# Kernel optimization log

Measured on AMD Instinct MI355X. Metric: run time of the kernel, lower is better.

The kernel has to match this reference:

```python
import jax, jax.numpy as jnp
import numpy as np

T, N, D = 64, 40, 4
H, R, K = 256, 64, 2
E = N * (N - 1)


def _xavier(key, shape):
    std = (2.0 / (shape[0] + shape[1])) ** 0.5
    return (std * jax.random.normal(key, shape)).astype(jnp.float32)


def setup_inputs() -> dict:
    ks = iter(jax.random.split(jax.random.key(0), 40))
    send, recv = np.where(np.ones((N, N)) - np.eye(N))  # fully-connected directed graph, E = N*(N-1)
    p = {}
    p['inputs'] = jax.random.normal(next(ks), (1, T, N, D), dtype=jnp.float32)
    p['node_masks'] = jnp.ones((1, T, N), dtype=jnp.float32)
    p['send_edges'] = jnp.asarray(send, dtype=jnp.int32)
    p['recv_edges'] = jnp.asarray(recv, dtype=jnp.int32)
    for name, nin in (('mlp1', D), ('mlp2', 2 * H), ('mlp3', H), ('mlp4', 3 * H)):
        p[name + '_W1'] = _xavier(next(ks), (H, nin))
        p[name + '_b1'] = jnp.full((H,), 0.1, jnp.float32)
        p[name + '_W2'] = _xavier(next(ks), (H, H))
        p[name + '_b2'] = jnp.full((H,), 0.1, jnp.float32)
    s = float(1.0 / np.sqrt(R))
    for nm in ('fwd', 'rev'):
        p[nm + '_Wih'] = jax.random.uniform(next(ks), (4 * R, H), jnp.float32, -s, s)
        p[nm + '_Whh'] = jax.random.uniform(next(ks), (4 * R, R), jnp.float32, -s, s)
        p[nm + '_bih'] = jnp.zeros((4 * R,), jnp.float32)
        p[nm + '_bhh'] = jnp.zeros((4 * R,), jnp.float32)
    p['enc_W'] = _xavier(next(ks), (K, 2 * R))
    p['enc_b'] = jnp.full((K,), 0.1, jnp.float32)
    p['prior_W'] = _xavier(next(ks), (K, R))
    p['prior_b'] = jnp.full((K,), 0.1, jnp.float32)
    return p


def _mlp(x, W1, b1, W2, b2):
    # RefNRIMLP in eval mode with no_bn=True: elu(fc2(elu(fc1(x))))
    return jax.nn.elu(jax.nn.elu(x @ W1.T + b1) @ W2.T + b2)


def _lstm(xs, Wih, Whh, bih, bhh):
    # xs: [T, E, H] -> hidden states [T, E, R]; PyTorch LSTM gate order i, f, g, o
    def step(carry, xt):
        h, c = carry
        g = xt @ Wih.T + bih + h @ Whh.T + bhh
        i, f, gg, o = jnp.split(g, 4, axis=-1)
        c = jax.nn.sigmoid(f) * c + jax.nn.sigmoid(i) * jnp.tanh(gg)
        h = jax.nn.sigmoid(o) * jnp.tanh(c)
        return (h, c), h
    Rh = Whh.shape[1]
    init = (jnp.zeros((xs.shape[1], Rh), xs.dtype), jnp.zeros((xs.shape[1], Rh), xs.dtype))
    _, hs = jax.lax.scan(step, init, xs)
    return hs


def _encode(inputs, send, recv,
            m1W1, m1b1, m1W2, m1b2, m2W1, m2b1, m2W2, m2b2,
            m3W1, m3b1, m3W2, m3b2, m4W1, m4b1, m4W2, m4b2,
            fWih, fWhh, fbih, fbhh, rWih, rWhh, rbih, rbhh,
            encW, encb, priW, prib):
    x = inputs[0]                                                  # [T, N, D]
    h = _mlp(x, m1W1, m1b1, m1W2, m1b2)                            # [T, N, H]
    e = jnp.concatenate([h[:, send], h[:, recv]], axis=-1)         # node2edge gather [T, E, 2H]
    e = _mlp(e, m2W1, m2b1, m2W2, m2b2)                            # [T, E, H]
    skip = e
    n = jnp.zeros((x.shape[0], x.shape[1], e.shape[-1]), e.dtype)
    n = n.at[:, recv].add(e)                                       # edge2node scatter-add (index_add_)
    n = _mlp(n, m3W1, m3b1, m3W2, m3b2)                            # [T, N, H]
    e = jnp.concatenate([n[:, send], n[:, recv], skip], axis=-1)   # [T, E, 3H]
    e = _mlp(e, m4W1, m4b1, m4W2, m4b2)                            # per-edge features over time [T, E, H]
    fwd_h = _lstm(e, fWih, fWhh, fbih, fbhh)                       # [T, E, R]
    rev_h = _lstm(e[::-1], rWih, rWhh, rbih, rbhh)[::-1]           # [T, E, R]
    prior = fwd_h @ priW.T + prib                                  # [T, E, K]
    enc = jnp.concatenate([fwd_h, rev_h], axis=-1) @ encW.T + encb # [T, E, K]
    return jnp.concatenate([prior, enc], axis=-1)                  # [T, E, 2K]


def reference(inputs, node_masks, send_edges, recv_edges,
              mlp1_W1, mlp1_b1, mlp1_W2, mlp1_b2,
              mlp2_W1, mlp2_b1, mlp2_W2, mlp2_b2,
              mlp3_W1, mlp3_b1, mlp3_W2, mlp3_b2,
              mlp4_W1, mlp4_b1, mlp4_W2, mlp4_b2,
              fwd_Wih, fwd_Whh, fwd_bih, fwd_bhh,
              rev_Wih, rev_Whh, rev_bih, rev_bhh,
              enc_W, enc_b, prior_W, prior_b):
    del node_masks  # all nodes present -> static fully-connected graph each step
    return _encode(inputs, send_edges, recv_edges,
                   mlp1_W1, mlp1_b1, mlp1_W2, mlp1_b2,
                   mlp2_W1, mlp2_b1, mlp2_W2, mlp2_b2,
                   mlp3_W1, mlp3_b1, mlp3_W2, mlp3_b2,
                   mlp4_W1, mlp4_b1, mlp4_W2, mlp4_b2,
                   fwd_Wih, fwd_Whh, fwd_bih, fwd_bhh,
                   rev_Wih, rev_Whh, rev_bih, rev_bhh,
                   enc_W, enc_b, prior_W, prior_b)
```

## Files before the change

kernel.cpp:

```cpp
#include <hip/hip_runtime.h>
#include <math.h>

#define T_ 64
#define N_ 40
#define D_ 4
#define H_ 256
#define R_ 64
#define E_ 1560
#define TE_ (T_*E_)
#define TN_ (T_*N_)

typedef unsigned short us;
typedef short short8 __attribute__((ext_vector_type(8)));
typedef float f32x4 __attribute__((ext_vector_type(4)));

__device__ __forceinline__ float elu_f(float x){ return x > 0.f ? x : (__expf(x) - 1.f); }
__device__ __forceinline__ float sig_f(float x){ return 1.f/(1.f+__expf(-x)); }
__device__ __forceinline__ float tanh_f(float x){ return 2.f/(1.f+__expf(-2.f*x)) - 1.f; }
__device__ __forceinline__ float dot4(float4 a, float4 b){ return a.x*b.x + a.y*b.y + a.z*b.z + a.w*b.w; }

__device__ __forceinline__ float bf2f(us u){ return __uint_as_float(((unsigned int)u) << 16); }
__device__ __forceinline__ us f2bf(float f){
    unsigned int u = __float_as_uint(f);
    u += 0x7FFFu + ((u >> 16) & 1u);
    return (us)(u >> 16);
}
__device__ __forceinline__ float4 ld4f(const float* p){ return *(const float4*)p; }
__device__ __forceinline__ float4 ld4f(const us* p){
    ushort4 v = *(const ushort4*)p;
    return make_float4(bf2f(v.x), bf2f(v.y), bf2f(v.z), bf2f(v.w));
}
__device__ __forceinline__ void st4f(float* p, float4 v){ *(float4*)p = v; }
__device__ __forceinline__ void st4f(us* p, float4 v){
    ushort4 o; o.x = f2bf(v.x); o.y = f2bf(v.y); o.z = f2bf(v.z); o.w = f2bf(v.w);
    *(ushort4*)p = o;
}

__device__ __forceinline__ void gld16(void* lds, const void* g){
    __builtin_amdgcn_global_load_lds((const __attribute__((address_space(1))) unsigned int*)g,
                                     (__attribute__((address_space(3))) unsigned int*)lds,
                                     16, 0, 0);
}

__device__ __forceinline__ void wsplit1(const float* W, us* hi, us* lo, int i){
    const float w = W[i];
    const us h = f2bf(w);
    hi[i] = h;
    lo[i] = f2bf(w - bf2f(h));
}

__global__ __launch_bounds__(256)
void wsplit_all(const float* __restrict__ s0, us* h0, us* l0,
                const float* __restrict__ s1, us* h1, us* l1,
                const float* __restrict__ s2, us* h2, us* l2,
                const float* __restrict__ s3, us* h3, us* l3,
                const float* __restrict__ s4, us* h4, us* l4,
                const float* __restrict__ s5, us* h5, us* l5,
                const float* __restrict__ s6, us* h6, us* l6)
{
    int i = blockIdx.x * 256 + threadIdx.x;
    if (i < 65536) { wsplit1(s0, h0, l0, i); return; } i -= 65536;
    if (i < 65536) {
        const float w = s1[(i >> 8) * 768 + 512 + (i & 255)];
        const us h = f2bf(w);
        h1[i] = h;
        l1[i] = f2bf(w - bf2f(h));
        return;
    } i -= 65536;
    if (i < 65536) { wsplit1(s2, h2, l2, i); return; } i -= 65536;
    if (i < 65536) { wsplit1(s3, h3, l3, i); return; } i -= 65536;
    if (i < 65536) { wsplit1(s4, h4, l4, i); return; } i -= 65536;
    if (i < 16384) { wsplit1(s5, h5, l5, i); return; } i -= 16384;
    wsplit1(s6, h6, l6, i);
}

__global__ __launch_bounds__(256)
void mlp1_kernel(const float* __restrict__ x,
                 const float* __restrict__ W1, const float* __restrict__ b1,
                 const float* __restrict__ W2, const float* __restrict__ b2,
                 us* __restrict__ hout)
{
    __shared__ float xs[8][4];
    __shared__ float h1[8][256];
    const int tid = threadIdx.x;
    const int r0  = blockIdx.x * 8;

    if (tid < 32) xs[tid >> 2][tid & 3] = x[r0 * 4 + tid];
    __syncthreads();

    const float4 w1 = *(const float4*)&W1[tid * 4];
    const float bb1 = b1[tid];
    #pragma unroll
    for (int row = 0; row < 8; ++row) {
        float v = bb1 + xs[row][0]*w1.x + xs[row][1]*w1.y + xs[row][2]*w1.z + xs[row][3]*w1.w;
        h1[row][tid] = elu_f(v);
    }
    __syncthreads();

    float acc[8];
    const float bb2 = b2[tid];
    #pragma unroll
    for (int row = 0; row < 8; ++row) acc[row] = bb2;
    const float* w2row = W2 + (size_t)tid * 256;
    for (int k4 = 0; k4 < 64; ++k4) {
        const float4 w = *(const float4*)&w2row[k4 * 4];
        #pragma unroll
        for (int row = 0; row < 8; ++row) {
            const float4 hh = *(const float4*)&h1[row][k4 * 4];
            acc[row] += dot4(hh, w);
        }
    }
    #pragma unroll
    for (int row = 0; row < 8; ++row)
        hout[(size_t)(r0 + row) * 256 + tid] = f2bf(elu_f(acc[row]));
}

__global__ __launch_bounds__(256)
void node_proj(const us* __restrict__ A, const float* __restrict__ W,
               int wstride, float* __restrict__ P)
{
    __shared__ float As[16][64];
    __shared__ float Ws[16][64];

    const int tid  = threadIdx.x;
    const int am   = tid >> 2;
    const int gm   = blockIdx.x * 64 + am;
    const int part = blockIdx.y >> 2;
    const int wq   = blockIdx.y & 3;

    const us* aptr = A + (size_t)gm * 256;
    const float* wptr = W + (size_t)(wq * 64 + am) * wstride + part * 256;

    const int tx = tid & 15, ty = tid >> 4;
    float acc[4][4] = {};

    for (int k0 = 0; k0 < 256; k0 += 16) {
        const float4 a4 = ld4f(aptr + k0 + (tid & 3) * 4);
        const float4 w4 = *(const float4*)(wptr + k0 + (tid & 3) * 4);

        __syncthreads();
        const int ak = (tid & 3) * 4;
        As[ak+0][am] = a4.x; As[ak+1][am] = a4.y; As[ak+2][am] = a4.z; As[ak+3][am] = a4.w;
        Ws[ak+0][am] = w4.x; Ws[ak+1][am] = w4.y; Ws[ak+2][am] = w4.z; Ws[ak+3][am] = w4.w;
        __syncthreads();

        #pragma unroll
        for (int kq = 0; kq < 16; ++kq) {
            const float4 av = *(const float4*)&As[kq][ty * 4];
            const float4 wv = *(const float4*)&Ws[kq][tx * 4];
            const float a_[4] = {av.x, av.y, av.z, av.w};
            const float w_[4] = {wv.x, wv.y, wv.z, wv.w};
            #pragma unroll
            for (int i = 0; i < 4; ++i)
                #pragma unroll
                for (int j = 0; j < 4; ++j)
                    acc[i][j] += a_[i] * w_[j];
        }
    }

    const int gn = part * 256 + wq * 64 + tx * 4;
    #pragma unroll
    for (int i = 0; i < 4; ++i) {
        const int row = blockIdx.x * 64 + ty * 4 + i;
        float4 o;
        o.x = acc[i][0]; o.y = acc[i][1]; o.z = acc[i][2]; o.w = acc[i][3];
        *(float4*)(P + (size_t)row * 512 + gn) = o;
    }
}

__global__ __launch_bounds__(256)
void edge_gather_elu(const float* __restrict__ P, const float* __restrict__ b1,
                     const int* __restrict__ send, const int* __restrict__ recv,
                     us* __restrict__ out)
{
    const int tid = threadIdx.x;
    const int r   = blockIdx.x * 4 + (tid >> 6);
    const int c4  = (tid & 63) * 4;
    const int t = r / E_;
    const int e = r - t * E_;
    const float4 a  = *(const float4*)(P + ((size_t)(t * N_ + send[e])) * 512 + c4);
    const float4 b  = *(const float4*)(P + ((size_t)(t * N_ + recv[e])) * 512 + 256 + c4);
    const float4 bb = *(const float4*)(b1 + c4);
    float4 v;
    v.x = elu_f(a.x + b.x + bb.x);
    v.y = elu_f(a.y + b.y + bb.y);
    v.z = elu_f(a.z + b.z + bb.z);
    v.w = elu_f(a.w + b.w + bb.w);
    ushort4 o; o.x = f2bf(v.x); o.y = f2bf(v.y); o.z = f2bf(v.z); o.w = f2bf(v.w);
    *(ushort4*)(out + (size_t)r * 256 + c4) = o;
}

template<int MODE, bool DOELU>
__global__ __launch_bounds__(256, 2)
void gemm_mfma(const us* __restrict__ A,
               const us* __restrict__ Whi, const us* __restrict__ Wlo,
               const float* __restrict__ bias1, const float* __restrict__ bias2,
               const int* __restrict__ send, const int* __restrict__ recv,
               const float* __restrict__ Ptab,
               us* __restrict__ C, int Kdim,
               const us* __restrict__ Whi2, const us* __restrict__ Wlo2,
               const float* __restrict__ bias1b, const float* __restrict__ bias2b,
               us* __restrict__ C2)
{
    __shared__ char smem[65536];

    const int tid  = threadIdx.x;
    const int lane = tid & 63;
    const int w    = tid >> 6;
    const int ml   = lane & 15;
    const int q    = lane >> 4;
    const int bx   = blockIdx.x;
    int by         = blockIdx.y;
    const int eh   = w >> 1;
    const int fh   = w & 1;

    if (MODE == 0 && C2 != nullptr && by >= 2) {
        Whi = Whi2; Wlo = Wlo2; bias1 = bias1b; bias2 = bias2b; C = C2; by -= 2;
    }

    const int lr   = lane >> 2;
    const int cofs = (((lane & 3) ^ ((lane >> 3) & 3)) * 8);

    const us* pA0[4];
    #pragma unroll
    for (int i = 0; i < 4; ++i) {
        const int gr = bx * 256 + i * 64 + w * 16 + lr;
        pA0[i] = A + (size_t)gr * Kdim;
    }
    const us *pWh[2], *pWl[2];
    #pragma unroll
    for (int j = 0; j < 2; ++j) {
        const int wr = by * 128 + j * 64 + w * 16 + lr;
        pWh[j] = Whi + (size_t)wr * Kdim;
        pWl[j] = Wlo + (size_t)wr * Kdim;
    }

    f32x4 acc[4][8];
    #pragma unroll
    for (int i = 0; i < 4; ++i)
        #pragma unroll
        for (int j = 0; j < 8; ++j)
            acc[i][j] = (f32x4){0.f, 0.f, 0.f, 0.f};

    auto stage = [&](int k0, char* base) {
        #pragma unroll
        for (int i = 0; i < 4; ++i)
            gld16(base + (i * 4 + w) * 1024, pA0[i] + k0 + cofs);
        #pragma unroll
        for (int j = 0; j < 2; ++j) {
            gld16(base + 16384 + (j * 4 + w) * 1024, pWh[j] + k0 + cofs);
            gld16(base + 24576 + (j * 4 + w) * 1024, pWl[j] + k0 + cofs);
        }
    };

    const int qs16 = (q ^ ((ml >> 1) & 3)) * 16;

    stage(0, smem);
    const int nk = Kdim >> 5;
    for (int k = 0; k < nk; ++k) {
        char* cur = smem + (k & 1) * 32768;
        char* nxt = smem + ((k + 1) & 1) * 32768;
        __builtin_amdgcn_s_barrier();
        if (k + 1 < nk) {
            stage((k + 1) * 32, nxt);
            __builtin_amdgcn_s_waitcnt(0x3F78);
        } else {
            __builtin_amdgcn_s_waitcnt(0x3F70);
        }
        __builtin_amdgcn_s_barrier();

        short8 wh[4], wl[4], ef[8];
        #pragma unroll
        for (int mt = 0; mt < 4; ++mt) {
            const int blkOf = (fh * 4 + mt) * 1024 + ml * 64 + qs16;
            wh[mt] = *(const short8*)(cur + 16384 + blkOf);
            wl[mt] = *(const short8*)(cur + 24576 + blkOf);
        }
        #pragma unroll
        for (int nt = 0; nt < 8; ++nt) {
            const int blkOf = (eh * 8 + nt) * 1024 + ml * 64 + qs16;
            ef[nt] = *(const short8*)(cur + blkOf);
        }
        #pragma unroll
        for (int nt = 0; nt < 8; ++nt)
            #pragma unroll
            for (int mt = 0; mt < 4; ++mt) {
                acc[mt][nt] = __builtin_amdgcn_mfma_f32_16x16x32_bf16(wh[mt], ef[nt], acc[mt][nt], 0, 0, 0);
                acc[mt][nt] = __builtin_amdgcn_mfma_f32_16x16x32_bf16(wl[mt], ef[nt], acc[mt][nt], 0, 0, 0);
            }
    }

    int srowA[8], rrowA[8];
    if (MODE == 3) {
        #pragma unroll
        for (int nt = 0; nt < 8; ++nt) {
            const int row = bx * 256 + eh * 128 + nt * 16 + ml;
            const int t = row / E_;
            const int e = row - t * E_;
            srowA[nt] = t * N_ + send[e];
            rrowA[nt] = t * N_ + recv[e];
        }
    }

    #pragma unroll
    for (int mt = 0; mt < 4; ++mt) {
        const int colb = by * 128 + fh * 64 + mt * 16 + q * 4;
        float4 bb = *(const float4*)(bias1 + colb);
        if (bias2) {
            const float4 b2 = *(const float4*)(bias2 + colb);
            bb.x += b2.x; bb.y += b2.y; bb.z += b2.z; bb.w += b2.w;
        }
        #pragma unroll
        for (int nt = 0; nt < 8; ++nt) {
            const int row = bx * 256 + eh * 128 + nt * 16 + ml;
            float4 v;
            v.x = acc[mt][nt][0] + bb.x; v.y = acc[mt][nt][1] + bb.y;
            v.z = acc[mt][nt][2] + bb.z; v.w = acc[mt][nt][3] + bb.w;
            if (MODE == 3) {
                const float4 pS = *(const float4*)(Ptab + (size_t)srowA[nt] * 512 + colb);
                const float4 pR = *(const float4*)(Ptab + (size_t)rrowA[nt] * 512 + 256 + colb);
                v.x += pS.x + pR.x; v.y += pS.y + pR.y;
                v.z += pS.z + pR.z; v.w += pS.w + pR.w;
            }
            if (DOELU) { v.x = elu_f(v.x); v.y = elu_f(v.y); v.z = elu_f(v.z); v.w = elu_f(v.w); }
            ushort4 o; o.x = f2bf(v.x); o.y = f2bf(v.y); o.z = f2bf(v.z); o.w = f2bf(v.w);
            *(ushort4*)(C + (size_t)row * 256 + colb) = o;
        }
    }
}

template<bool DOELU, typename TA, typename TC>
__global__ __launch_bounds__(256)
void gemm_nt(const TA* __restrict__ A, const float* __restrict__ W,
             const float* __restrict__ bias1,
             TC* __restrict__ C, int M, int Kdim)
{
    __shared__ float As[16][64];
    __shared__ float Ws[16][64];

    const int tid = threadIdx.x;
    const int am  = tid >> 2;
    const int ak  = (tid & 3) * 4;
    const int gm  = blockIdx.x * 64 + am;

    const TA* aptr0 = A + (size_t)gm * Kdim;
    const float* wptr = W + (size_t)(blockIdx.y * 64 + am) * Kdim;

    const int tx = tid & 15, ty = tid >> 4;
    float acc[4][4] = {};

    for (int k0 = 0; k0 < Kdim; k0 += 16) {
        const float4 a4 = ld4f(aptr0 + k0 + ak);
        const float4 w4 = *(const float4*)(wptr + k0 + (tid & 3) * 4);

        __syncthreads();
        As[ak+0][am] = a4.x; As[ak+1][am] = a4.y; As[ak+2][am] = a4.z; As[ak+3][am] = a4.w;
        const int wk = (tid & 3) * 4;
        Ws[wk+0][am] = w4.x; Ws[wk+1][am] = w4.y; Ws[wk+2][am] = w4.z; Ws[wk+3][am] = w4.w;
        __syncthreads();

        #pragma unroll
        for (int kq = 0; kq < 16; ++kq) {
            const float4 av = *(const float4*)&As[kq][ty * 4];
            const float4 wv = *(const float4*)&Ws[kq][tx * 4];
            const float a_[4] = {av.x, av.y, av.z, av.w};
            const float w_[4] = {wv.x, wv.y, wv.z, wv.w};
            #pragma unroll
            for (int i = 0; i < 4; ++i)
                #pragma unroll
                for (int j = 0; j < 4; ++j)
                    acc[i][j] += a_[i] * w_[j];
        }
    }

    const int gn = blockIdx.y * 64 + tx * 4;
    const float4 bb = *(const float4*)&bias1[gn];
    #pragma unroll
    for (int i = 0; i < 4; ++i) {
        const int row = blockIdx.x * 64 + ty * 4 + i;
        float4 o;
        o.x = acc[i][0] + bb.x; o.y = acc[i][1] + bb.y;
        o.z = acc[i][2] + bb.z; o.w = acc[i][3] + bb.w;
        if (DOELU) { o.x = elu_f(o.x); o.y = elu_f(o.y); o.z = elu_f(o.z); o.w = elu_f(o.w); }
        st4f(C + (size_t)row * 256 + gn, o);
    }
}

__global__ __launch_bounds__(256)
void aggregate_kernel(const us* __restrict__ eSkip, const int* __restrict__ recv,
                      float* __restrict__ nAgg)
{
    const int t = blockIdx.x / N_;
    const int j = blockIdx.x - t * N_;
    const int c = threadIdx.x;
    const us* basep = eSkip + (size_t)t * E_ * H_ + c;
    float acc = 0.f;
    #pragma unroll
    for (int s = 0; s < N_; ++s) {
        if (s == j) continue;
        const int e = s * (N_ - 1) + (j < s ? j : j - 1);
        acc += bf2f(basep[(size_t)e * H_]);
    }
    nAgg[(size_t)blockIdx.x * H_ + c] = acc;
}

__global__ __launch_bounds__(256)
void lstm_mfma(const us* __restrict__ Gf, const us* __restrict__ Gr,
               const us* __restrict__ fWhhH, const us* __restrict__ fWhhL,
               const us* __restrict__ rWhhH, const us* __restrict__ rWhhL,
               float* __restrict__ hsF, float* __restrict__ hsR)
{
    const int NBD = (E_ + 15) / 16;
    const bool revd = (int)blockIdx.x >= NBD;
    const int blk = revd ? (int)blockIdx.x - NBD : (int)blockIdx.x;
    const int e0 = blk * 16;
    const us* G  = revd ? Gr : Gf;
    const us* WH = revd ? rWhhH : fWhhH;
    const us* WL = revd ? rWhhL : fWhhL;
    float* hs    = revd ? hsR : hsF;

    const int tid  = threadIdx.x;
    const int lane = tid & 63;
    const int w    = tid >> 6;
    const int ml   = lane & 15;
    const int q    = lane >> 4;

    __shared__ us hHi[2][16][72];
    __shared__ us hLo[2][16][72];

    short8 wfh[4][2], wfl[4][2];
    #pragma unroll
    for (int mt = 0; mt < 4; ++mt) {
        const int row = mt * 64 + w * 16 + ml;
        #pragma unroll
        for (int ks = 0; ks < 2; ++ks) {
            wfh[mt][ks] = *(const short8*)(WH + (size_t)row * 64 + ks * 32 + q * 8);
            wfl[mt][ks] = *(const short8*)(WL + (size_t)row * 64 + ks * 32 + q * 8);
        }
    }

    for (int i = tid; i < 16 * 72; i += 256) { (&hHi[0][0][0])[i] = 0; (&hLo[0][0][0])[i] = 0; }

    const int eMF = min(e0 + ml, E_ - 1);
    const bool wr = (e0 + ml) < E_;
    const int gOfs = w * 16 + q * 4;
    float4 cst = make_float4(0.f, 0.f, 0.f, 0.f);

    ushort4 gcur[4], gnxt[4];
    {
        const int tt0 = revd ? (T_ - 1) : 0;
        const us* gp = G + ((size_t)tt0 * E_ + eMF) * 256 + gOfs;
        #pragma unroll
        for (int mt = 0; mt < 4; ++mt) gcur[mt] = *(const ushort4*)(gp + mt * 64);
    }
    __syncthreads();

    for (int s = 0; s < T_; ++s) {
        const int tt = revd ? (T_ - 1 - s) : s;
        {
            const int sn = (s + 1 < T_) ? s + 1 : s;
            const int tn = revd ? (T_ - 1 - sn) : sn;
            const us* gp = G + ((size_t)tn * E_ + eMF) * 256 + gOfs;
            #pragma unroll
            for (int mt = 0; mt < 4; ++mt) gnxt[mt] = *(const ushort4*)(gp + mt * 64);
        }
        const int rb = s & 1, wb = rb ^ 1;
        short8 bh[2], bl[2];
        #pragma unroll
        for (int ks = 0; ks < 2; ++ks) {
            bh[ks] = *(const short8*)(&hHi[rb][ml][ks * 32 + q * 8]);
            bl[ks] = *(const short8*)(&hLo[rb][ml][ks * 32 + q * 8]);
        }
        f32x4 acc[4];
        #pragma unroll
        for (int mt = 0; mt < 4; ++mt) {
            acc[mt][0] = bf2f(gcur[mt].x); acc[mt][1] = bf2f(gcur[mt].y);
            acc[mt][2] = bf2f(gcur[mt].z); acc[mt][3] = bf2f(gcur[mt].w);
            #pragma unroll
            for (int ks = 0; ks < 2; ++ks) {
                acc[mt] = __builtin_amdgcn_mfma_f32_16x16x32_bf16(wfh[mt][ks], bh[ks], acc[mt], 0, 0, 0);
                acc[mt] = __builtin_amdgcn_mfma_f32_16x16x32_bf16(wfh[mt][ks], bl[ks], acc[mt], 0, 0, 0);
                acc[mt] = __builtin_amdgcn_mfma_f32_16x16x32_bf16(wfl[mt][ks], bh[ks], acc[mt], 0, 0, 0);
            }
        }
        float4 hv;
        cst.x = sig_f(acc[1][0])*cst.x + sig_f(acc[0][0])*tanh_f(acc[2][0]); hv.x = sig_f(acc[3][0])*tanh_f(cst.x);
        cst.y = sig_f(acc[1][1])*cst.y + sig_f(acc[0][1])*tanh_f(acc[2][1]); hv.y = sig_f(acc[3][1])*tanh_f(cst.y);
        cst.z = sig_f(acc[1][2])*cst.z + sig_f(acc[0][2])*tanh_f(acc[2][2]); hv.z = sig_f(acc[3][2])*tanh_f(cst.z);
        cst.w = sig_f(acc[1][3])*cst.w + sig_f(acc[0][3])*tanh_f(acc[2][3]); hv.w = sig_f(acc[3][3])*tanh_f(cst.w);
        ushort4 hh4, hl4;
        hh4.x = f2bf(hv.x); hl4.x = f2bf(hv.x - bf2f(hh4.x));
        hh4.y = f2bf(hv.y); hl4.y = f2bf(hv.y - bf2f(hh4.y));
        hh4.z = f2bf(hv.z); hl4.z = f2bf(hv.z - bf2f(hh4.z));
        hh4.w = f2bf(hv.w); hl4.w = f2bf(hv.w - bf2f(hh4.w));
        *(ushort4*)(&hHi[wb][ml][gOfs]) = hh4;
        *(ushort4*)(&hLo[wb][ml][gOfs]) = hl4;
        if (wr)
            *(float4*)(&hs[((size_t)tt * E_ + e0 + ml) * 64 + gOfs]) = hv;
        __syncthreads();
        #pragma unroll
        for (int mt = 0; mt < 4; ++mt) gcur[mt] = gnxt[mt];
    }
}

__global__ __launch_bounds__(256)
void out_kernel(const float* __restrict__ hsF, const float* __restrict__ hsR,
                const float* __restrict__ priW, const float* __restrict__ prib,
                const float* __restrict__ encW, const float* __restrict__ encb,
                float* __restrict__ out)
{
    const int idx = blockIdx.x * 256 + threadIdx.x;
    const float* f = hsF + (size_t)idx * 64;
    const float* r = hsR + (size_t)idx * 64;
    float p0 = prib[0], p1 = prib[1], q0 = encb[0], q1 = encb[1];
    #pragma unroll
    for (int k4 = 0; k4 < 16; ++k4) {
        const float4 fv = *(const float4*)(f + k4 * 4);
        const float4 rv = *(const float4*)(r + k4 * 4);
        p0 += dot4(fv, *(const float4*)(priW + k4 * 4));
        p1 += dot4(fv, *(const float4*)(priW + 64 + k4 * 4));
        q0 += dot4(fv, *(const float4*)(encW + k4 * 4))
            + dot4(rv, *(const float4*)(encW + 64 + k4 * 4));
        q1 += dot4(fv, *(const float4*)(encW + 128 + k4 * 4))
            + dot4(rv, *(const float4*)(encW + 192 + k4 * 4));
    }
    float4 o; o.x = p0; o.y = p1; o.z = q0; o.w = q1;
    *(float4*)(out + (size_t)idx * 4) = o;
}

extern "C" void kernel_launch(void* const* d_in, const int* in_sizes, int n_in,
                              void* d_out, int out_size, void* d_ws, size_t ws_size,
                              hipStream_t stream)
{
    const float* x    = (const float*)d_in[0];
    const int*   send = (const int*)d_in[2];
    const int*   recv = (const int*)d_in[3];
    const float* m1W1 = (const float*)d_in[4];  const float* m1b1 = (const float*)d_in[5];
    const float* m1W2 = (const float*)d_in[6];  const float* m1b2 = (const float*)d_in[7];
    const float* m2W1 = (const float*)d_in[8];  const float* m2b1 = (const float*)d_in[9];
    const float* m2W2 = (const float*)d_in[10]; const float* m2b2 = (const float*)d_in[11];
    const float* m3W1 = (const float*)d_in[12]; const float* m3b1 = (const float*)d_in[13];
    const float* m3W2 = (const float*)d_in[14]; const float* m3b2 = (const float*)d_in[15];
    const float* m4W1 = (const float*)d_in[16]; const float* m4b1 = (const float*)d_in[17];
    const float* m4W2 = (const float*)d_in[18]; const float* m4b2 = (const float*)d_in[19];
    const float* fWih = (const float*)d_in[20]; const float* fWhh = (const float*)d_in[21];
    const float* fbih = (const float*)d_in[22]; const float* fbhh = (const float*)d_in[23];
    const float* rWih = (const float*)d_in[24]; const float* rWhh = (const float*)d_in[25];
    const float* rbih = (const float*)d_in[26]; const float* rbhh = (const float*)d_in[27];
    const float* encW = (const float*)d_in[28]; const float* encb = (const float*)d_in[29];
    const float* priW = (const float*)d_in[30]; const float* prib = (const float*)d_in[31];

    const size_t SZN  = (size_t)TN_ * H_;
    const size_t SZE  = (size_t)TE_ * H_;
    float* n_agg = (float*)d_ws;
    float* m3t   = n_agg + SZN;
    float* Ptab  = (float*)d_ws;
    us* h16      = (us*)(m3t + SZN);
    us* n3       = h16 + SZN;
    us* w2bH = n3  + SZN;          us* w2bL = w2bH + 65536;
    us* w4aH = w2bL + 65536;       us* w4aL = w4aH + 65536;
    us* w4bH = w4aL + 65536;       us* w4bL = w4bH + 65536;
    us* wfiH = w4bL + 65536;       us* wfiL = wfiH + 65536;
    us* wriH = wfiL + 65536;       us* wriL = wriH + 65536;
    us* whfH = wriL + 65536;       us* whfL = whfH + 16384;
    us* whrH = whfL + 16384;       us* whrL = whrH + 16384;
    us* bufA16 = whrL + 16384;
    us* bufB16 = bufA16 + SZE;
    us* bufC16 = bufB16 + SZE;
    float* hsF = (float*)bufC16;
    float* hsR = hsF + (size_t)TE_ * R_;
    const size_t needed = ((size_t)(bufC16 + SZE) - (size_t)d_ws);
    if (ws_size < needed) return;

    const dim3 gMF(TE_ / 256, 2), gMF4(TE_ / 256, 4), gN(TN_ / 64, 4), gNP(TN_ / 64, 8);
    const us* z = nullptr; const float* zf = nullptr; us* zo = nullptr;

    wsplit_all<<<1408, 256, 0, stream>>>(m2W2, w2bH, w2bL,
                                         m4W1, w4aH, w4aL,
                                         m4W2, w4bH, w4bL,
                                         fWih, wfiH, wfiL, rWih, wriH, wriL,
                                         fWhh, whfH, whfL, rWhh, whrH, whrL);

    mlp1_kernel<<<TN_ / 8, 256, 0, stream>>>(x, m1W1, m1b1, m1W2, m1b2, h16);
    node_proj<<<gNP, 256, 0, stream>>>(h16, m2W1, 512, Ptab);
    edge_gather_elu<<<TE_ / 4, 256, 0, stream>>>(Ptab, m2b1, send, recv, bufA16);
    gemm_mfma<0, true><<<gMF, 256, 0, stream>>>(bufA16, w2bH, w2bL, m2b2, nullptr, send, recv, zf, bufB16, 256, z, z, zf, zf, zo);
    aggregate_kernel<<<TN_, 256, 0, stream>>>(bufB16, recv, n_agg);
    gemm_nt<true, float, float><<<gN, 256, 0, stream>>>(n_agg, m3W1, m3b1, m3t, TN_, 256);
    gemm_nt<true, float, us><<<gN, 256, 0, stream>>>(m3t, m3W2, m3b2, n3, TN_, 256);
    node_proj<<<gNP, 256, 0, stream>>>(n3, m4W1, 768, Ptab);
    gemm_mfma<3, true><<<gMF, 256, 0, stream>>>(bufB16, w4aH, w4aL, m4b1, nullptr, send, recv, Ptab, bufA16, 256, z, z, zf, zf, zo);
    gemm_mfma<0, true><<<gMF, 256, 0, stream>>>(bufA16, w4bH, w4bL, m4b2, nullptr, send, recv, zf, bufC16, 256, z, z, zf, zf, zo);
    gemm_mfma<0, false><<<gMF4, 256, 0, stream>>>(bufC16, wfiH, wfiL, fbih, fbhh, send, recv, zf, bufA16, 256,
                                                  wriH, wriL, rbih, rbhh, bufB16);
    lstm_mfma<<<2 * ((E_ + 15) / 16), 256, 0, stream>>>(bufA16, bufB16, whfH, whfL, whrH, whrL, hsF, hsR);
    out_kernel<<<TE_ / 256, 256, 0, stream>>>(hsF, hsR, priW, prib, encW, encb, (float*)d_out);
}
```

Before: 568.4 us.

## Widen MFMA GEMM block to 512 threads covering all 256 output columns

The edge GEMM kernel now uses 8 waves per block, and each block computes a full 256x256 output tile instead of a 256x128 tile. The grid's y dimension is halved, so each A tile is loaded once rather than twice, and LDS grows to 96KB double-buffered. It also raises wave priority around the MFMA loop with s_setprio. The trade-off is fewer blocks (about 390 per GEMM), larger LDS per block and possibly lower occupancy.

```diff
diff --git a/kernel.cpp b/kernel.cpp
--- a/kernel.cpp
+++ b/kernel.cpp
@@ -191,7 +191,7 @@
 }
 
 template<int MODE, bool DOELU>
-__global__ __launch_bounds__(256, 2)
+__global__ __launch_bounds__(512, 2)
 void gemm_mfma(const us* __restrict__ A,
                const us* __restrict__ Whi, const us* __restrict__ Wlo,
                const float* __restrict__ bias1, const float* __restrict__ bias2,
@@ -202,7 +202,7 @@
                const float* __restrict__ bias1b, const float* __restrict__ bias2b,
                us* __restrict__ C2)
 {
-    __shared__ char smem[65536];
+    __shared__ char smem[98304];
 
     const int tid  = threadIdx.x;
     const int lane = tid & 63;
@@ -210,29 +210,24 @@
     const int ml   = lane & 15;
     const int q    = lane >> 4;
     const int bx   = blockIdx.x;
-    int by         = blockIdx.y;
-    const int eh   = w >> 1;
-    const int fh   = w & 1;
-
-    if (MODE == 0 && C2 != nullptr && by >= 2) {
-        Whi = Whi2; Wlo = Wlo2; bias1 = bias1b; bias2 = bias2b; C = C2; by -= 2;
-    }
+
+    if (MODE == 0 && C2 != nullptr && blockIdx.y == 1) {
+        Whi = Whi2; Wlo = Wlo2; bias1 = bias1b; bias2 = bias2b; C = C2;
+    }
+
+    const int eh = w >> 2;
+    const int fh = w & 3;
 
     const int lr   = lane >> 2;
     const int cofs = (((lane & 3) ^ ((lane >> 3) & 3)) * 8);
 
-    const us* pA0[4];
-    #pragma unroll
-    for (int i = 0; i < 4; ++i) {
-        const int gr = bx * 256 + i * 64 + w * 16 + lr;
-        pA0[i] = A + (size_t)gr * Kdim;
-    }
-    const us *pWh[2], *pWl[2];
-    #pragma unroll
-    for (int j = 0; j < 2; ++j) {
-        const int wr = by * 128 + j * 64 + w * 16 + lr;
-        pWh[j] = Whi + (size_t)wr * Kdim;
-        pWl[j] = Wlo + (size_t)wr * Kdim;
+    const us *pA[2], *pWh[2], *pWl[2];
+    #pragma unroll
+    for (int i = 0; i < 2; ++i) {
+        const int r = w * 32 + i * 16 + lr;
+        pA[i]  = A   + (size_t)(bx * 256 + r) * Kdim;
+        pWh[i] = Whi + (size_t)r * Kdim;
+        pWl[i] = Wlo + (size_t)r * Kdim;
     }
 
     f32x4 acc[4][8];
@@ -244,12 +239,10 @@
 
     auto stage = [&](int k0, char* base) {
         #pragma unroll
-        for (int i = 0; i < 4; ++i)
-            gld16(base + (i * 4 + w) * 1024, pA0[i] + k0 + cofs);
-        #pragma unroll
-        for (int j = 0; j < 2; ++j) {
-            gld16(base + 16384 + (j * 4 + w) * 1024, pWh[j] + k0 + cofs);
-            gld16(base + 24576 + (j * 4 + w) * 1024, pWl[j] + k0 + cofs);
+        for (int i = 0; i < 2; ++i) {
+            gld16(base +         (w * 2 + i) * 1024, pA[i]  + k0 + cofs);
+            gld16(base + 16384 + (w * 2 + i) * 1024, pWh[i] + k0 + cofs);
+            gld16(base + 32768 + (w * 2 + i) * 1024, pWl[i] + k0 + cofs);
         }
     };
 
@@ -258,12 +251,12 @@
     stage(0, smem);
     const int nk = Kdim >> 5;
     for (int k = 0; k < nk; ++k) {
-        char* cur = smem + (k & 1) * 32768;
-        char* nxt = smem + ((k + 1) & 1) * 32768;
+        char* cur = smem + (k & 1) * 49152;
+        char* nxt = smem + ((k + 1) & 1) * 49152;
         __builtin_amdgcn_s_barrier();
         if (k + 1 < nk) {
             stage((k + 1) * 32, nxt);
-            __builtin_amdgcn_s_waitcnt(0x3F78);
+            __builtin_amdgcn_s_waitcnt(0x3F76);
         } else {
             __builtin_amdgcn_s_waitcnt(0x3F70);
         }
@@ -274,13 +267,14 @@
         for (int mt = 0; mt < 4; ++mt) {
             const int blkOf = (fh * 4 + mt) * 1024 + ml * 64 + qs16;
             wh[mt] = *(const short8*)(cur + 16384 + blkOf);
-            wl[mt] = *(const short8*)(cur + 24576 + blkOf);
+            wl[mt] = *(const short8*)(cur + 32768 + blkOf);
         }
         #pragma unroll
         for (int nt = 0; nt < 8; ++nt) {
             const int blkOf = (eh * 8 + nt) * 1024 + ml * 64 + qs16;
             ef[nt] = *(const short8*)(cur + blkOf);
         }
+        __builtin_amdgcn_s_setprio(1);
         #pragma unroll
         for (int nt = 0; nt < 8; ++nt)
             #pragma unroll
@@ -288,6 +282,7 @@
                 acc[mt][nt] = __builtin_amdgcn_mfma_f32_16x16x32_bf16(wh[mt], ef[nt], acc[mt][nt], 0, 0, 0);
                 acc[mt][nt] = __builtin_amdgcn_mfma_f32_16x16x32_bf16(wl[mt], ef[nt], acc[mt][nt], 0, 0, 0);
             }
+        __builtin_amdgcn_s_setprio(0);
     }
 
     int srowA[8], rrowA[8];
@@ -304,7 +299,7 @@
 
     #pragma unroll
     for (int mt = 0; mt < 4; ++mt) {
-        const int colb = by * 128 + fh * 64 + mt * 16 + q * 4;
+        const int colb = fh * 64 + mt * 16 + q * 4;
         float4 bb = *(const float4*)(bias1 + colb);
         if (bias2) {
             const float4 b2 = *(const float4*)(bias2 + colb);
@@ -572,7 +567,7 @@
     const size_t needed = ((size_t)(bufC16 + SZE) - (size_t)d_ws);
     if (ws_size < needed) return;
 
-    const dim3 gMF(TE_ / 256, 2), gMF4(TE_ / 256, 4), gN(TN_ / 64, 4), gNP(TN_ / 64, 8);
+    const dim3 gMF(TE_ / 256, 1), gMFd(TE_ / 256, 2), gN(TN_ / 64, 4), gNP(TN_ / 64, 8);
     const us* z = nullptr; const float* zf = nullptr; us* zo = nullptr;
 
     wsplit_all<<<1408, 256, 0, stream>>>(m2W2, w2bH, w2bL,
@@ -584,14 +579,14 @@
     mlp1_kernel<<<TN_ / 8, 256, 0, stream>>>(x, m1W1, m1b1, m1W2, m1b2, h16);
     node_proj<<<gNP, 256, 0, stream>>>(h16, m2W1, 512, Ptab);
     edge_gather_elu<<<TE_ / 4, 256, 0, stream>>>(Ptab, m2b1, send, recv, bufA16);
-    gemm_mfma<0, true><<<gMF, 256, 0, stream>>>(bufA16, w2bH, w2bL, m2b2, nullptr, send, recv, zf, bufB16, 256, z, z, zf, zf, zo);
+    gemm_mfma<0, true><<<gMF, 512, 0, stream>>>(bufA16, w2bH, w2bL, m2b2, nullptr, send, recv, zf, bufB16, 256, z, z, zf, zf, zo);
     aggregate_kernel<<<TN_, 256, 0, stream>>>(bufB16, recv, n_agg);
     gemm_nt<true, float, float><<<gN, 256, 0, stream>>>(n_agg, m3W1, m3b1, m3t, TN_, 256);
     gemm_nt<true, float, us><<<gN, 256, 0, stream>>>(m3t, m3W2, m3b2, n3, TN_, 256);
     node_proj<<<gNP, 256, 0, stream>>>(n3, m4W1, 768, Ptab);
-    gemm_mfma<3, true><<<gMF, 256, 0, stream>>>(bufB16, w4aH, w4aL, m4b1, nullptr, send, recv, Ptab, bufA16, 256, z, z, zf, zf, zo);
-    gemm_mfma<0, true><<<gMF, 256, 0, stream>>>(bufA16, w4bH, w4bL, m4b2, nullptr, send, recv, zf, bufC16, 256, z, z, zf, zf, zo);
-    gemm_mfma<0, false><<<gMF4, 256, 0, stream>>>(bufC16, wfiH, wfiL, fbih, fbhh, send, recv, zf, bufA16, 256,
+    gemm_mfma<3, true><<<gMF, 512, 0, stream>>>(bufB16, w4aH, w4aL, m4b1, nullptr, send, recv, Ptab, bufA16, 256, z, z, zf, zf, zo);
+    gemm_mfma<0, true><<<gMF, 512, 0, stream>>>(bufA16, w4bH, w4bL, m4b2, nullptr, send, recv, zf, bufC16, 256, z, z, zf, zf, zo);
+    gemm_mfma<0, false><<<gMFd, 512, 0, stream>>>(bufC16, wfiH, wfiL, fbih, fbhh, send, recv, zf, bufA16, 256,
                                                   wriH, wriL, rbih, rbhh, bufB16);
     lstm_mfma<<<2 * ((E_ + 15) / 16), 256, 0, stream>>>(bufA16, bufB16, whfH, whfL, whrH, whrL, hsF, hsR);
     out_kernel<<<TE_ / 256, 256, 0, stream>>>(hsF, hsR, priW, prib, encW, encb, (float*)d_out);
```

New measurement: 586.2 us. +3.1%, slower.
